# Kernel tuning notes

Measured on AMD Instinct MI355X. Metric: run time of the kernel, lower is better.

Reference implementation:

```python
import jax, jax.numpy as jnp
import numpy as np

K_HEADS = 8
D_HEAD = 64
D = K_HEADS * D_HEAD  # 512
B, TP, TQ, N = 8, 48, 48, 256


def setup_inputs() -> dict:
    key = jax.random.key(0)
    ks = jax.random.split(key, 13)
    s = 1.0 / np.sqrt(D)
    inp = {
        "X": jax.random.normal(ks[0], (B, TP, N, D), jnp.float32),
        "STE_P": jax.random.normal(ks[1], (B, TP, N, D), jnp.float32),
        "STE_Q": jax.random.normal(ks[2], (B, TQ, N, D), jnp.float32),
        "Wq": jax.random.uniform(ks[3], (D, D), jnp.float32, -s, s),
        "bq": jax.random.uniform(ks[4], (D,), jnp.float32, -s, s),
        "Wk": jax.random.uniform(ks[5], (D, D), jnp.float32, -s, s),
        "bk": jax.random.uniform(ks[6], (D,), jnp.float32, -s, s),
        "Wv": jax.random.uniform(ks[7], (D, D), jnp.float32, -s, s),
        "bv": jax.random.uniform(ks[8], (D,), jnp.float32, -s, s),
        "W1": jax.random.uniform(ks[9], (D, D), jnp.float32, -s, s),
        "b1": jax.random.uniform(ks[10], (D,), jnp.float32, -s, s),
        "W2": jax.random.uniform(ks[11], (D, D), jnp.float32, -s, s),
        "b2": jax.random.uniform(ks[12], (D,), jnp.float32, -s, s),
    }
    return inp


def reference(X, STE_P, STE_Q, Wq, bq, Wk, bk, Wv, bv, W1, b1, W2, b2):
    # ReLU-fused QKV projections
    q = jax.nn.relu(STE_Q @ Wq + bq)  # [B, Tq, N, D]
    k = jax.nn.relu(STE_P @ Wk + bk)  # [B, Tp, N, D]
    v = jax.nn.relu(X @ Wv + bv)      # [B, Tp, N, D]

    # split(last, d) + cat(dim 0) == introduce head axis h of size K
    b, tq, n, _ = q.shape
    tp = k.shape[1]
    q = q.reshape(b, tq, n, K_HEADS, D_HEAD)
    k = k.reshape(b, tp, n, K_HEADS, D_HEAD)
    v = v.reshape(b, tp, n, K_HEADS, D_HEAD)

    # attention over the TIME axis, per node and head: scores [b,h,n,tq,tp]
    scale = 1.0 / jnp.sqrt(jnp.asarray(D_HEAD, q.dtype))
    attn = jnp.einsum('bqnhd,bpnhd->bhnqp', q, k) * scale
    attn = jax.nn.softmax(attn, axis=-1)
    out = jnp.einsum('bhnqp,bpnhd->bqnhd', attn, v).reshape(b, tq, n, D)

    out = jax.nn.relu(out @ W1 + b1) @ W2 + b2
    return out
```

## Files before the change

### kernel.cpp

```cpp
#include <hip/hip_runtime.h>

typedef _Float16 f16;
typedef __fp16 hf2 __attribute__((ext_vector_type(2)));
typedef _Float16 f16x4 __attribute__((ext_vector_type(4)));
typedef _Float16 f16x8 __attribute__((ext_vector_type(8)));
typedef float f32x4 __attribute__((ext_vector_type(4)));

typedef const __attribute__((address_space(1))) unsigned int guint;
typedef __attribute__((address_space(3))) unsigned int luint;
__device__ __forceinline__ void gl_lds16(const void* g, void* l) {
    __builtin_amdgcn_global_load_lds((guint*)g, (luint*)l, 16, 0, 0);
}
template <int N>
__device__ __forceinline__ void vmwait() {
    if constexpr (N == 8)       asm volatile("s_waitcnt vmcnt(8)" ::: "memory");
    else if constexpr (N == 6)  asm volatile("s_waitcnt vmcnt(6)" ::: "memory");
    else if constexpr (N == 4)  asm volatile("s_waitcnt vmcnt(4)" ::: "memory");
    else                        asm volatile("s_waitcnt vmcnt(0)" ::: "memory");
}
__device__ __forceinline__ void barrier_raw() { __builtin_amdgcn_s_barrier(); __builtin_amdgcn_sched_barrier(0); }
__device__ __forceinline__ void lgkm0() { asm volatile("s_waitcnt lgkmcnt(0)" ::: "memory"); }

__device__ __forceinline__ f16x8 pack8(float4 x0, float4 x1) {
    hf2 p0 = __builtin_amdgcn_cvt_pkrtz(x0.x, x0.y);
    hf2 p1 = __builtin_amdgcn_cvt_pkrtz(x0.z, x0.w);
    hf2 p2 = __builtin_amdgcn_cvt_pkrtz(x1.x, x1.y);
    hf2 p3 = __builtin_amdgcn_cvt_pkrtz(x1.z, x1.w);
    f16x8 h;
    h[0] = (f16)p0[0]; h[1] = (f16)p0[1]; h[2] = (f16)p1[0]; h[3] = (f16)p1[1];
    h[4] = (f16)p2[0]; h[5] = (f16)p2[1]; h[6] = (f16)p3[0]; h[7] = (f16)p3[1];
    return h;
}

__global__ __launch_bounds__(256) void wconv(const float* w0, const float* w1, const float* w2,
                                             const float* w3, const float* w4, f16* dst) {
    const float* src;
    switch (blockIdx.z) { case 0: src = w0; break; case 1: src = w1; break;
                          case 2: src = w2; break; case 3: src = w3; break; default: src = w4; }
    __shared__ float tile[32][33];
    int k0 = blockIdx.x * 32, n0 = blockIdx.y * 32;
    int t = threadIdx.x;
    int r = t >> 3, c4 = (t & 7) * 4;
    float4 v = *(const float4*)(src + (k0 + r) * 512 + n0 + c4);
    tile[r][c4 + 0] = v.x; tile[r][c4 + 1] = v.y; tile[r][c4 + 2] = v.z; tile[r][c4 + 3] = v.w;
    __syncthreads();
    f16x4 o;
    o[0] = (f16)tile[c4 + 0][r]; o[1] = (f16)tile[c4 + 1][r];
    o[2] = (f16)tile[c4 + 2][r]; o[3] = (f16)tile[c4 + 3][r];
    *(f16x4*)(dst + (size_t)blockIdx.z * 262144 + (n0 + r) * 512 + k0 + c4) = o;
}

__global__ __launch_bounds__(512, 2) void gemm_rs(const float* __restrict__ A,
                                                  const f16* __restrict__ Bt,
                                                  const float* __restrict__ bias,
                                                  f16* __restrict__ Cp) {
    constexpr int BUFSZ = 32768;
    __shared__ __align__(16) char smem[4 * BUFSZ];

    const int cpx = gridDim.x >> 3;
    const int orig = blockIdx.x;
    const int wgid = (orig & 7) * cpx + (orig >> 3);
    const int by = wgid & 1, bx = wgid >> 1;
    const int r0 = bx * 256, c0 = by * 256;

    const int t = threadIdx.x, j = t & 63, w = t >> 6;
    const int lr = j & 15, lq = j >> 4;
    const int wr = (w >> 2) * 128, wc = (w & 3) * 64;

    const float* aS = A + (size_t)(r0 + (t >> 1)) * 512 + (t & 1) * 16;
    const int awRow = t >> 1;
    const int awS = (t >> 2) & 3;
    const int awc = (t & 1) * 2;
    const int aw0 = awRow * 64 + ((awc ^ awS) << 4);
    const int aw1 = awRow * 64 + (((awc + 1) ^ awS) << 4);

    const int srow = t >> 2;
    const int sblk = (t & 3) ^ ((t >> 3) & 3);
    const f16* bS = Bt + (size_t)(c0 + srow) * 512 + sblk * 8;
    const int dstT = t * 16;

    int aoff[8], boff[4];
#pragma unroll
    for (int m = 0; m < 8; m++) {
        int row = wr + m * 16 + lr;
        aoff[m] = row * 64 + ((lq ^ ((row >> 1) & 3)) << 4);
    }
#pragma unroll
    for (int nb = 0; nb < 4; nb++) {
        int row = wc + nb * 16 + lr;
        boff[nb] = 16384 + row * 64 + ((lq ^ ((row >> 1) & 3)) << 4);
    }

    f32x4 acc[8][4] = {};
    float4 rgA[4], rgB[4];

    auto loadTo = [&](int kt, float4* rg) {
        const float* p = aS + kt * 32;
        rg[0] = *(const float4*)p;
        rg[1] = *(const float4*)(p + 4);
        rg[2] = *(const float4*)(p + 8);
        rg[3] = *(const float4*)(p + 12);
    };
    auto writeA = [&](const float4* rg, int buf) {
        char* base = smem + buf * BUFSZ;
        *(f16x8*)(base + aw0) = pack8(rg[0], rg[1]);
        *(f16x8*)(base + aw1) = pack8(rg[2], rg[3]);
    };
    auto stageB = [&](int kt) {
        char* d = smem + (kt & 3) * BUFSZ + 16384 + dstT;
        const f16* s = bS + kt * 32;
        gl_lds16(s, d);
        gl_lds16(s + 65536, d + 8192);
    };

#define PHASE_A(kt, bfr)                                                    \
    do {                                                                    \
        const char* sb_ = smem + ((kt) & 3) * BUFSZ;                        \
        f16x8 afr[4];                                                       \
        _Pragma("unroll")                                                   \
        for (int nb = 0; nb < 4; nb++) bfr[nb] = *(const f16x8*)(sb_ + boff[nb]); \
        _Pragma("unroll")                                                   \
        for (int m = 0; m < 4; m++) afr[m] = *(const f16x8*)(sb_ + aoff[m]); \
        __builtin_amdgcn_s_setprio(1);                                      \
        _Pragma("unroll")                                                   \
        for (int m = 0; m < 4; m++)                                         \
            _Pragma("unroll")                                               \
            for (int nb = 0; nb < 4; nb++)                                  \
                acc[m][nb] = __builtin_amdgcn_mfma_f32_16x16x32_f16(afr[m], bfr[nb], acc[m][nb], 0, 0, 0); \
        __builtin_amdgcn_s_setprio(0);                                      \
    } while (0)

#define PHASE_B(kt, bfr)                                                    \
    do {                                                                    \
        const char* sb_ = smem + ((kt) & 3) * BUFSZ;                        \
        f16x8 afr2[4];                                                      \
        _Pragma("unroll")                                                   \
        for (int m = 0; m < 4; m++) afr2[m] = *(const f16x8*)(sb_ + aoff[m + 4]); \
        __builtin_amdgcn_s_setprio(1);                                      \
        _Pragma("unroll")                                                   \
        for (int m = 0; m < 4; m++)                                         \
            _Pragma("unroll")                                               \
            for (int nb = 0; nb < 4; nb++)                                  \
                acc[m + 4][nb] = __builtin_amdgcn_mfma_f32_16x16x32_f16(afr2[m], bfr[nb], acc[m + 4][nb], 0, 0, 0); \
        __builtin_amdgcn_s_setprio(0);                                      \
    } while (0)

    loadTo(0, rgA);
    stageB(0); stageB(1);
    loadTo(1, rgB);
    stageB(2);
    vmwait<8>();
    __builtin_amdgcn_sched_barrier(0);
    writeA(rgA, 0);
    lgkm0();
    barrier_raw();

#pragma unroll 1
    for (int k2 = 0; k2 < 8; ++k2) {
        {
            const int kt = 2 * k2;
            if (k2 <= 6) loadTo(kt + 2, rgA);
            if (k2 <= 6) vmwait<6>(); else vmwait<0>();
            __builtin_amdgcn_sched_barrier(0);
            writeA(rgB, (kt + 1) & 3);
            f16x8 bfr[4];
            PHASE_A(kt, bfr);
            barrier_raw();
            if (k2 <= 6) stageB(kt + 3);
            PHASE_B(kt, bfr);
            lgkm0();
            barrier_raw();
        }
        {
            const int kt = 2 * k2 + 1;
            if (k2 <= 6) loadTo(kt + 2, rgB);
            if (k2 <= 6) vmwait<6>(); else vmwait<0>();
            __builtin_amdgcn_sched_barrier(0);
            if (k2 <= 6) writeA(rgA, (kt + 1) & 3);
            f16x8 bfr[4];
            PHASE_A(kt, bfr);
            barrier_raw();
            if (k2 <= 5) stageB(kt + 3);
            PHASE_B(kt, bfr);
            lgkm0();
            barrier_raw();
        }
    }
#undef PHASE_A
#undef PHASE_B

#pragma unroll
    for (int nb = 0; nb < 4; nb++) {
        int col = c0 + wc + nb * 16 + lr;
        float b = bias[col];
#pragma unroll
        for (int m = 0; m < 8; m++) {
#pragma unroll
            for (int r = 0; r < 4; r++) {
                float v = fmaxf(acc[m][nb][r] + b, 0.0f);
                size_t row = (size_t)(r0 + wr + m * 16 + lq * 4 + r);
                Cp[row * 512 + col] = (f16)v;
            }
        }
    }
}

template <bool RELU, bool O16>
__global__ __launch_bounds__(512, 2) void gemm_8ph(const f16* __restrict__ A,
                                                   const f16* __restrict__ Bt,
                                                   const float* __restrict__ bias,
                                                   void* __restrict__ Cp) {
    constexpr int BUFSZ = 32768;
    __shared__ __align__(16) char smem[4 * BUFSZ];

    const int cpx = gridDim.x >> 3;
    const int orig = blockIdx.x;
    const int wgid = (orig & 7) * cpx + (orig >> 3);
    const int by = wgid & 1;
    const int bx = wgid >> 1;
    const int r0 = bx * 256, c0 = by * 256;

    const int t = threadIdx.x;
    const int j = t & 63, w = t >> 6;
    const int lr = j & 15, lq = j >> 4;
    const int wr = (w >> 2) * 128, wc = (w & 3) * 64;

    const int srow = t >> 2;
    const int sblk = (t & 3) ^ ((t >> 3) & 3);
    const f16* aS = A  + (size_t)(r0 + srow) * 512 + sblk * 8;
    const f16* bS = Bt + (size_t)(c0 + srow) * 512 + sblk * 8;
    const int dstT = t * 16;

    int aoff[8], boff[4];
#pragma unroll
    for (int m = 0; m < 8; m++) {
        int row = wr + m * 16 + lr;
        aoff[m] = row * 64 + ((lq ^ ((row >> 1) & 3)) << 4);
    }
#pragma unroll
    for (int nb = 0; nb < 4; nb++) {
        int row = wc + nb * 16 + lr;
        boff[nb] = 16384 + row * 64 + ((lq ^ ((row >> 1) & 3)) << 4);
    }

    f32x4 acc[8][4] = {};

    auto stageA = [&](int kt) {
        char* d = smem + (kt & 3) * BUFSZ + dstT;
        const f16* s = aS + kt * 32;
        gl_lds16(s, d);
        gl_lds16(s + 65536, d + 8192);
    };
    auto stageB = [&](int kt) {
        char* d = smem + (kt & 3) * BUFSZ + 16384 + dstT;
        const f16* s = bS + kt * 32;
        gl_lds16(s, d);
        gl_lds16(s + 65536, d + 8192);
    };

    stageA(0); stageB(0); stageA(1); stageB(1); stageA(2); stageB(2);

#pragma unroll 1
    for (int kt = 0; kt < 16; ++kt) {
        const char* sb = smem + (kt & 3) * BUFSZ;
        if (kt <= 13)      vmwait<8>();
        else if (kt == 14) vmwait<4>();
        else               vmwait<0>();
        barrier_raw();
        if (kt < 13) stageA(kt + 3);
        f16x8 bfr[4], afr[4];
#pragma unroll
        for (int nb = 0; nb < 4; nb++) bfr[nb] = *(const f16x8*)(sb + boff[nb]);
#pragma unroll
        for (int m = 0; m < 4; m++) afr[m] = *(const f16x8*)(sb + aoff[m]);
        __builtin_amdgcn_s_setprio(1);
#pragma unroll
        for (int m = 0; m < 4; m++)
#pragma unroll
            for (int nb = 0; nb < 4; nb++)
                acc[m][nb] = __builtin_amdgcn_mfma_f32_16x16x32_f16(afr[m], bfr[nb], acc[m][nb], 0, 0, 0);
        __builtin_amdgcn_s_setprio(0);
        barrier_raw();
        if (kt < 13) stageB(kt + 3);
        f16x8 afr2[4];
#pragma unroll
        for (int m = 0; m < 4; m++) afr2[m] = *(const f16x8*)(sb + aoff[m + 4]);
        __builtin_amdgcn_s_setprio(1);
#pragma unroll
        for (int m = 0; m < 4; m++)
#pragma unroll
            for (int nb = 0; nb < 4; nb++)
                acc[m + 4][nb] = __builtin_amdgcn_mfma_f32_16x16x32_f16(afr2[m], bfr[nb], acc[m + 4][nb], 0, 0, 0);
        __builtin_amdgcn_s_setprio(0);
    }

#pragma unroll
    for (int nb = 0; nb < 4; nb++) {
        int col = c0 + wc + nb * 16 + lr;
        float b = bias[col];
#pragma unroll
        for (int m = 0; m < 8; m++) {
#pragma unroll
            for (int r = 0; r < 4; r++) {
                float v = acc[m][nb][r] + b;
                if (RELU) v = fmaxf(v, 0.0f);
                size_t row = (size_t)(r0 + wr + m * 16 + lq * 4 + r);
                if (O16) ((f16*)Cp)[row * 512 + col] = (f16)v;
                else     ((float*)Cp)[row * 512 + col] = v;
            }
        }
    }
}

__global__ __launch_bounds__(64) void attn_kernel(const f16* __restrict__ q,
                                                  const f16* __restrict__ k,
                                                  const f16* __restrict__ v,
                                                  f16* __restrict__ out) {
    const int h = blockIdx.x, n = blockIdx.y, b = blockIdx.z;
    __shared__ f16 sQ[48 * 72];
    __shared__ f16 sK[48 * 72];
    __shared__ f16 sP[48 * 72];
    __shared__ f16 sVt[64 * 72];
    const int l = threadIdx.x, lr = l & 15, lq = l >> 4;
    const size_t rowstride = 256 * 512;
    const size_t base = ((size_t)(b * 48) * 256 + n) * 512 + h * 64;

    const int pr = l >> 3, pc = (l & 7) * 8;
#pragma unroll
    for (int pass = 0; pass < 6; pass++) {
        int row = pass * 8 + pr;
        size_t g = base + (size_t)row * rowstride + pc;
        f16x8 qv = *(const f16x8*)(q + g);
        f16x8 kv = *(const f16x8*)(k + g);
        f16x8 vv = *(const f16x8*)(v + g);
        *(f16x8*)&sQ[row * 72 + pc] = qv;
        *(f16x8*)&sK[row * 72 + pc] = kv;
#pragma unroll
        for (int jj = 0; jj < 8; jj++) sVt[(pc + jj) * 72 + row] = vv[jj];
    }
    {
        f16x8 z = {};
        *(f16x8*)&sVt[l * 72 + 48] = z;
        *(f16x8*)&sVt[l * 72 + 56] = z;
        if (l < 48) { *(f16x8*)&sP[l * 72 + 48] = z; *(f16x8*)&sP[l * 72 + 56] = z; }
    }
    __syncthreads();

    f32x4 s[3][3] = {};
#pragma unroll
    for (int ks = 0; ks < 2; ks++) {
        f16x8 aq[3], bk[3];
#pragma unroll
        for (int m = 0; m < 3; m++)  aq[m] = *(const f16x8*)&sQ[(m * 16 + lr) * 72 + ks * 32 + lq * 8];
#pragma unroll
        for (int nb = 0; nb < 3; nb++) bk[nb] = *(const f16x8*)&sK[(nb * 16 + lr) * 72 + ks * 32 + lq * 8];
#pragma unroll
        for (int m = 0; m < 3; m++)
#pragma unroll
            for (int nb = 0; nb < 3; nb++)
                s[m][nb] = __builtin_amdgcn_mfma_f32_16x16x32_f16(aq[m], bk[nb], s[m][nb], 0, 0, 0);
    }

#pragma unroll
    for (int m = 0; m < 3; m++) {
#pragma unroll
        for (int r = 0; r < 4; r++) {
            float a0 = s[m][0][r] * 0.125f, a1 = s[m][1][r] * 0.125f, a2 = s[m][2][r] * 0.125f;
            float mx = fmaxf(a0, fmaxf(a1, a2));
#pragma unroll
            for (int d = 1; d < 16; d <<= 1) mx = fmaxf(mx, __shfl_xor(mx, d));
            float e0 = __expf(a0 - mx), e1 = __expf(a1 - mx), e2 = __expf(a2 - mx);
            float sm = e0 + e1 + e2;
#pragma unroll
            for (int d = 1; d < 16; d <<= 1) sm += __shfl_xor(sm, d);
            float inv = 1.0f / sm;
            int row = m * 16 + lq * 4 + r;
            sP[row * 72 + 0  + lr] = (f16)(e0 * inv);
            sP[row * 72 + 16 + lr] = (f16)(e1 * inv);
            sP[row * 72 + 32 + lr] = (f16)(e2 * inv);
        }
    }
    __syncthreads();

    f32x4 o[3][4] = {};
#pragma unroll
    for (int ks = 0; ks < 2; ks++) {
        f16x8 ap[3], bvv[4];
#pragma unroll
        for (int m = 0; m < 3; m++)  ap[m] = *(const f16x8*)&sP[(m * 16 + lr) * 72 + ks * 32 + lq * 8];
#pragma unroll
        for (int nb = 0; nb < 4; nb++) bvv[nb] = *(const f16x8*)&sVt[(nb * 16 + lr) * 72 + ks * 32 + lq * 8];
#pragma unroll
        for (int m = 0; m < 3; m++)
#pragma unroll
            for (int nb = 0; nb < 4; nb++)
                o[m][nb] = __builtin_amdgcn_mfma_f32_16x16x32_f16(ap[m], bvv[nb], o[m][nb], 0, 0, 0);
    }

#pragma unroll
    for (int m = 0; m < 3; m++)
#pragma unroll
        for (int nb = 0; nb < 4; nb++)
#pragma unroll
            for (int r = 0; r < 4; r++) {
                int row = m * 16 + lq * 4 + r;
                out[base + (size_t)row * rowstride + nb * 16 + lr] = (f16)o[m][nb][r];
            }
}

extern "C" void kernel_launch(void* const* d_in, const int* in_sizes, int n_in,
                              void* d_out, int out_size, void* d_ws, size_t ws_size,
                              hipStream_t stream) {
    const float* X    = (const float*)d_in[0];
    const float* STEP = (const float*)d_in[1];
    const float* STEQ = (const float*)d_in[2];
    const float* Wq   = (const float*)d_in[3];
    const float* bq   = (const float*)d_in[4];
    const float* Wk   = (const float*)d_in[5];
    const float* bk   = (const float*)d_in[6];
    const float* Wv   = (const float*)d_in[7];
    const float* bv   = (const float*)d_in[8];
    const float* W1   = (const float*)d_in[9];
    const float* b1   = (const float*)d_in[10];
    const float* W2   = (const float*)d_in[11];
    const float* b2   = (const float*)d_in[12];
    float* out = (float*)d_out;

    const size_t MROWS = 98304;
    const size_t MBUF  = MROWS * 512;
    f16* ws  = (f16*)d_ws;
    f16* Wqt = ws;
    f16* Wkt = ws + 262144;
    f16* Wvt = ws + 524288;
    f16* W1t = ws + 786432;
    f16* W2t = ws + 1048576;
    f16* qb  = ws + 1310720;
    f16* kb  = qb + MBUF;
    f16* vb  = kb + MBUF;
    f16* hb  = kb;

    wconv<<<dim3(16, 16, 5), 256, 0, stream>>>(Wq, Wk, Wv, W1, W2, ws);

    gemm_rs<<<768, 512, 0, stream>>>(STEQ, Wqt, bq, qb);
    gemm_rs<<<768, 512, 0, stream>>>(STEP, Wkt, bk, kb);
    gemm_rs<<<768, 512, 0, stream>>>(X,    Wvt, bv, vb);

    attn_kernel<<<dim3(8, 256, 8), 64, 0, stream>>>(qb, kb, vb, qb);

    gemm_8ph<true,  true ><<<768, 512, 0, stream>>>(qb, W1t, b1, hb);
    gemm_8ph<false, false><<<768, 512, 0, stream>>>(hb, W2t, b2, out);
}
```

Before: 610.7 us.

## Deepen A-operand register prefetch to three stages in QKV GEMM

The A tile (fp32 activations loaded into registers, then converted to fp16 and written to LDS) now uses three rotating register buffers instead of two, so global loads are issued three k-steps ahead. The main loop is restructured into groups of three sub-iterations with adjusted vmcnt waits and a peeled final step. This is meant to hide more global-load latency in the projection GEMM, at the cost of extra VGPRs that could reduce occupancy or cause spills.

```diff
diff --git a/kernel.cpp b/kernel.cpp
--- a/kernel.cpp
+++ b/kernel.cpp
@@ -13,9 +13,11 @@
 }
 template <int N>
 __device__ __forceinline__ void vmwait() {
-    if constexpr (N == 8)       asm volatile("s_waitcnt vmcnt(8)" ::: "memory");
+    if constexpr (N == 12)      asm volatile("s_waitcnt vmcnt(12)" ::: "memory");
+    else if constexpr (N == 8)  asm volatile("s_waitcnt vmcnt(8)" ::: "memory");
     else if constexpr (N == 6)  asm volatile("s_waitcnt vmcnt(6)" ::: "memory");
     else if constexpr (N == 4)  asm volatile("s_waitcnt vmcnt(4)" ::: "memory");
+    else if constexpr (N == 2)  asm volatile("s_waitcnt vmcnt(2)" ::: "memory");
     else                        asm volatile("s_waitcnt vmcnt(0)" ::: "memory");
 }
 __device__ __forceinline__ void barrier_raw() { __builtin_amdgcn_s_barrier(); __builtin_amdgcn_sched_barrier(0); }
@@ -92,7 +94,7 @@
     }
 
     f32x4 acc[8][4] = {};
-    float4 rgA[4], rgB[4];
+    float4 rg0[4], rg1[4], rg2[4];
 
     auto loadTo = [&](int kt, float4* rg) {
         const float* p = aS + kt * 32;
@@ -145,47 +147,47 @@
         __builtin_amdgcn_s_setprio(0);                                      \
     } while (0)
 
-    loadTo(0, rgA);
-    stageB(0); stageB(1);
-    loadTo(1, rgB);
-    stageB(2);
-    vmwait<8>();
+#define SUBITER(kt, RL, RW)                                                 \
+    do {                                                                    \
+        if ((kt) <= 12) loadTo((kt) + 3, RL);                               \
+        if ((kt) <= 12)      vmwait<12>();                                  \
+        else if ((kt) == 13) vmwait<8>();                                   \
+        else                 vmwait<2>();                                   \
+        __builtin_amdgcn_sched_barrier(0);                                  \
+        writeA(RW, ((kt) + 1) & 3);                                         \
+        f16x8 bfr[4];                                                       \
+        PHASE_A((kt), bfr);                                                 \
+        barrier_raw();                                                      \
+        if ((kt) <= 12) stageB((kt) + 3);                                   \
+        PHASE_B((kt), bfr);                                                 \
+        lgkm0();                                                            \
+        barrier_raw();                                                      \
+    } while (0)
+
+    loadTo(0, rg0); stageB(0);
+    loadTo(1, rg1); stageB(1);
+    loadTo(2, rg2); stageB(2);
+    vmwait<12>();
     __builtin_amdgcn_sched_barrier(0);
-    writeA(rgA, 0);
+    writeA(rg0, 0);
     lgkm0();
     barrier_raw();
 
 #pragma unroll 1
-    for (int k2 = 0; k2 < 8; ++k2) {
-        {
-            const int kt = 2 * k2;
-            if (k2 <= 6) loadTo(kt + 2, rgA);
-            if (k2 <= 6) vmwait<6>(); else vmwait<0>();
-            __builtin_amdgcn_sched_barrier(0);
-            writeA(rgB, (kt + 1) & 3);
-            f16x8 bfr[4];
-            PHASE_A(kt, bfr);
-            barrier_raw();
-            if (k2 <= 6) stageB(kt + 3);
-            PHASE_B(kt, bfr);
-            lgkm0();
-            barrier_raw();
-        }
-        {
-            const int kt = 2 * k2 + 1;
-            if (k2 <= 6) loadTo(kt + 2, rgB);
-            if (k2 <= 6) vmwait<6>(); else vmwait<0>();
-            __builtin_amdgcn_sched_barrier(0);
-            if (k2 <= 6) writeA(rgA, (kt + 1) & 3);
-            f16x8 bfr[4];
-            PHASE_A(kt, bfr);
-            barrier_raw();
-            if (k2 <= 5) stageB(kt + 3);
-            PHASE_B(kt, bfr);
-            lgkm0();
-            barrier_raw();
-        }
-    }
+    for (int k3 = 0; k3 < 5; ++k3) {
+        const int kt = k3 * 3;
+        SUBITER(kt,     rg0, rg1);
+        SUBITER(kt + 1, rg1, rg2);
+        SUBITER(kt + 2, rg2, rg0);
+    }
+    vmwait<0>();
+    barrier_raw();
+    {
+        f16x8 bfr[4];
+        PHASE_A(15, bfr);
+        PHASE_B(15, bfr);
+    }
+#undef SUBITER
 #undef PHASE_A
 #undef PHASE_B
 
```

Result: slower. 699.1 us (+14.5%).

## Shrink QKV projection GEMM tiles to 128x128 with triple-buffered pipeline

Applied to the files above, without the earlier changes.

The fp32-input QKV projection GEMM moves from 256x256 tiles with 512 threads and four LDS buffers to 128x128 tiles with 256 threads, three rotating LDS buffers, and three workgroups per CU. The grid grows from 768 to 3072 blocks per projection, and the K loop gains an explicit epilogue with a new vmcnt(2) wait. The aim is higher occupancy and better latency hiding on this load-bound kernel. In exchange, each tile reuses its data less, so total global/L2 traffic for A and B rises.

```diff
diff --git a/kernel.cpp b/kernel.cpp
--- a/kernel.cpp
+++ b/kernel.cpp
@@ -16,6 +16,7 @@
     if constexpr (N == 8)       asm volatile("s_waitcnt vmcnt(8)" ::: "memory");
     else if constexpr (N == 6)  asm volatile("s_waitcnt vmcnt(6)" ::: "memory");
     else if constexpr (N == 4)  asm volatile("s_waitcnt vmcnt(4)" ::: "memory");
+    else if constexpr (N == 2)  asm volatile("s_waitcnt vmcnt(2)" ::: "memory");
     else                        asm volatile("s_waitcnt vmcnt(0)" ::: "memory");
 }
 __device__ __forceinline__ void barrier_raw() { __builtin_amdgcn_s_barrier(); __builtin_amdgcn_sched_barrier(0); }
@@ -50,22 +51,23 @@
     *(f16x4*)(dst + (size_t)blockIdx.z * 262144 + (n0 + r) * 512 + k0 + c4) = o;
 }
 
-__global__ __launch_bounds__(512, 2) void gemm_rs(const float* __restrict__ A,
-                                                  const f16* __restrict__ Bt,
-                                                  const float* __restrict__ bias,
-                                                  f16* __restrict__ Cp) {
-    constexpr int BUFSZ = 32768;
-    __shared__ __align__(16) char smem[4 * BUFSZ];
+__global__ __launch_bounds__(256, 3) void gemm_rs3(const float* __restrict__ A,
+                                                   const f16* __restrict__ Bt,
+                                                   const float* __restrict__ bias,
+                                                   f16* __restrict__ Cp) {
+    constexpr int ASZ = 8192;
+    constexpr int BUFSZ = 16384;
+    __shared__ __align__(16) char smem[3 * BUFSZ];
 
     const int cpx = gridDim.x >> 3;
     const int orig = blockIdx.x;
     const int wgid = (orig & 7) * cpx + (orig >> 3);
-    const int by = wgid & 1, bx = wgid >> 1;
-    const int r0 = bx * 256, c0 = by * 256;
+    const int by = wgid & 3, bx = wgid >> 2;
+    const int r0 = bx * 128, c0 = by * 128;
 
     const int t = threadIdx.x, j = t & 63, w = t >> 6;
     const int lr = j & 15, lq = j >> 4;
-    const int wr = (w >> 2) * 128, wc = (w & 3) * 64;
+    const int wr = (w >> 1) * 64, wc = (w & 1) * 64;
 
     const float* aS = A + (size_t)(r0 + (t >> 1)) * 512 + (t & 1) * 16;
     const int awRow = t >> 1;
@@ -79,19 +81,19 @@
     const f16* bS = Bt + (size_t)(c0 + srow) * 512 + sblk * 8;
     const int dstT = t * 16;
 
-    int aoff[8], boff[4];
-#pragma unroll
-    for (int m = 0; m < 8; m++) {
+    int aoff[4], boff[4];
+#pragma unroll
+    for (int m = 0; m < 4; m++) {
         int row = wr + m * 16 + lr;
         aoff[m] = row * 64 + ((lq ^ ((row >> 1) & 3)) << 4);
     }
 #pragma unroll
     for (int nb = 0; nb < 4; nb++) {
         int row = wc + nb * 16 + lr;
-        boff[nb] = 16384 + row * 64 + ((lq ^ ((row >> 1) & 3)) << 4);
-    }
-
-    f32x4 acc[8][4] = {};
+        boff[nb] = ASZ + row * 64 + ((lq ^ ((row >> 1) & 3)) << 4);
+    }
+
+    f32x4 acc[4][4] = {};
     float4 rgA[4], rgB[4];
 
     auto loadTo = [&](int kt, float4* rg) {
@@ -106,85 +108,105 @@
         *(f16x8*)(base + aw0) = pack8(rg[0], rg[1]);
         *(f16x8*)(base + aw1) = pack8(rg[2], rg[3]);
     };
-    auto stageB = [&](int kt) {
-        char* d = smem + (kt & 3) * BUFSZ + 16384 + dstT;
+    auto stageB = [&](int kt, int buf) {
+        char* d = smem + buf * BUFSZ + ASZ + dstT;
         const f16* s = bS + kt * 32;
         gl_lds16(s, d);
-        gl_lds16(s + 65536, d + 8192);
+        gl_lds16(s + 32768, d + 4096);
     };
 
-#define PHASE_A(kt, bfr)                                                    \
+#define PHASE_A(buf, bfr)                                                   \
     do {                                                                    \
-        const char* sb_ = smem + ((kt) & 3) * BUFSZ;                        \
-        f16x8 afr[4];                                                       \
+        const char* sb_ = smem + (buf) * BUFSZ;                             \
+        f16x8 afr[2];                                                       \
         _Pragma("unroll")                                                   \
         for (int nb = 0; nb < 4; nb++) bfr[nb] = *(const f16x8*)(sb_ + boff[nb]); \
         _Pragma("unroll")                                                   \
-        for (int m = 0; m < 4; m++) afr[m] = *(const f16x8*)(sb_ + aoff[m]); \
+        for (int m = 0; m < 2; m++) afr[m] = *(const f16x8*)(sb_ + aoff[m]); \
         __builtin_amdgcn_s_setprio(1);                                      \
         _Pragma("unroll")                                                   \
-        for (int m = 0; m < 4; m++)                                         \
+        for (int m = 0; m < 2; m++)                                         \
             _Pragma("unroll")                                               \
             for (int nb = 0; nb < 4; nb++)                                  \
                 acc[m][nb] = __builtin_amdgcn_mfma_f32_16x16x32_f16(afr[m], bfr[nb], acc[m][nb], 0, 0, 0); \
         __builtin_amdgcn_s_setprio(0);                                      \
     } while (0)
 
-#define PHASE_B(kt, bfr)                                                    \
+#define PHASE_B(buf, bfr)                                                   \
     do {                                                                    \
-        const char* sb_ = smem + ((kt) & 3) * BUFSZ;                        \
-        f16x8 afr2[4];                                                      \
+        const char* sb_ = smem + (buf) * BUFSZ;                             \
+        f16x8 afr2[2];                                                      \
         _Pragma("unroll")                                                   \
-        for (int m = 0; m < 4; m++) afr2[m] = *(const f16x8*)(sb_ + aoff[m + 4]); \
+        for (int m = 0; m < 2; m++) afr2[m] = *(const f16x8*)(sb_ + aoff[m + 2]); \
         __builtin_amdgcn_s_setprio(1);                                      \
         _Pragma("unroll")                                                   \
-        for (int m = 0; m < 4; m++)                                         \
+        for (int m = 0; m < 2; m++)                                         \
             _Pragma("unroll")                                               \
             for (int nb = 0; nb < 4; nb++)                                  \
-                acc[m + 4][nb] = __builtin_amdgcn_mfma_f32_16x16x32_f16(afr2[m], bfr[nb], acc[m + 4][nb], 0, 0, 0); \
+                acc[m + 2][nb] = __builtin_amdgcn_mfma_f32_16x16x32_f16(afr2[m], bfr[nb], acc[m + 2][nb], 0, 0, 0); \
         __builtin_amdgcn_s_setprio(0);                                      \
     } while (0)
 
-    loadTo(0, rgA);
-    stageB(0); stageB(1);
-    loadTo(1, rgB);
-    stageB(2);
-    vmwait<8>();
+    loadTo(0, rgA); stageB(0, 0);
+    loadTo(1, rgB); stageB(1, 1);
+    vmwait<6>();
     __builtin_amdgcn_sched_barrier(0);
     writeA(rgA, 0);
     lgkm0();
     barrier_raw();
 
+    int bc = 0, bn = 1, b2 = 2;
 #pragma unroll 1
-    for (int k2 = 0; k2 < 8; ++k2) {
+    for (int k2 = 0; k2 < 7; ++k2) {
         {
             const int kt = 2 * k2;
-            if (k2 <= 6) loadTo(kt + 2, rgA);
-            if (k2 <= 6) vmwait<6>(); else vmwait<0>();
-            __builtin_amdgcn_sched_barrier(0);
-            writeA(rgB, (kt + 1) & 3);
+            loadTo(kt + 2, rgA);
+            vmwait<6>();
+            barrier_raw();
+            writeA(rgB, bn);
             f16x8 bfr[4];
-            PHASE_A(kt, bfr);
-            barrier_raw();
-            if (k2 <= 6) stageB(kt + 3);
-            PHASE_B(kt, bfr);
+            PHASE_A(bc, bfr);
+            barrier_raw();
+            stageB(kt + 2, b2);
+            PHASE_B(bc, bfr);
             lgkm0();
             barrier_raw();
+            int tmp = bc; bc = bn; bn = b2; b2 = tmp;
         }
         {
             const int kt = 2 * k2 + 1;
-            if (k2 <= 6) loadTo(kt + 2, rgB);
-            if (k2 <= 6) vmwait<6>(); else vmwait<0>();
-            __builtin_amdgcn_sched_barrier(0);
-            if (k2 <= 6) writeA(rgA, (kt + 1) & 3);
+            loadTo(kt + 2, rgB);
+            vmwait<6>();
+            barrier_raw();
+            writeA(rgA, bn);
             f16x8 bfr[4];
-            PHASE_A(kt, bfr);
-            barrier_raw();
-            if (k2 <= 5) stageB(kt + 3);
-            PHASE_B(kt, bfr);
+            PHASE_A(bc, bfr);
+            barrier_raw();
+            stageB(kt + 2, b2);
+            PHASE_B(bc, bfr);
             lgkm0();
             barrier_raw();
+            int tmp = bc; bc = bn; bn = b2; b2 = tmp;
         }
+    }
+    {
+        vmwait<2>();
+        barrier_raw();
+        writeA(rgB, bn);
+        f16x8 bfr[4];
+        PHASE_A(bc, bfr);
+        barrier_raw();
+        PHASE_B(bc, bfr);
+        lgkm0();
+        barrier_raw();
+        int tmp = bc; bc = bn; bn = b2; b2 = tmp;
+    }
+    {
+        vmwait<0>();
+        barrier_raw();
+        f16x8 bfr[4];
+        PHASE_A(bc, bfr);
+        PHASE_B(bc, bfr);
     }
 #undef PHASE_A
 #undef PHASE_B
@@ -194,7 +216,7 @@
         int col = c0 + wc + nb * 16 + lr;
         float b = bias[col];
 #pragma unroll
-        for (int m = 0; m < 8; m++) {
+        for (int m = 0; m < 4; m++) {
 #pragma unroll
             for (int r = 0; r < 4; r++) {
                 float v = fmaxf(acc[m][nb][r] + b, 0.0f);
@@ -441,9 +463,9 @@
 
     wconv<<<dim3(16, 16, 5), 256, 0, stream>>>(Wq, Wk, Wv, W1, W2, ws);
 
-    gemm_rs<<<768, 512, 0, stream>>>(STEQ, Wqt, bq, qb);
-    gemm_rs<<<768, 512, 0, stream>>>(STEP, Wkt, bk, kb);
-    gemm_rs<<<768, 512, 0, stream>>>(X,    Wvt, bv, vb);
+    gemm_rs3<<<3072, 256, 0, stream>>>(STEQ, Wqt, bq, qb);
+    gemm_rs3<<<3072, 256, 0, stream>>>(STEP, Wkt, bk, kb);
+    gemm_rs3<<<3072, 256, 0, stream>>>(X,    Wvt, bv, vb);
 
     attn_kernel<<<dim3(8, 256, 8), 64, 0, stream>>>(qb, kb, vb, qb);
 
```

Result: slower. 631.7 us (+3.4%).
